# Kernel tuning notes

Hardware: AMD Instinct MI355X
Metric: run time of the kernel (lower is better)

## Reference

```python
import jax, jax.numpy as jnp
import numpy as np


def setup_inputs() -> dict:
    key = jax.random.key(0)
    ks = jax.random.split(key, 6)
    b, t, s, qu, vu, d = 8, 64, 512, 512, 512, 512
    return {
        "query": jax.random.normal(ks[0], (b, t, qu), jnp.float32),
        "value": jax.random.normal(ks[1], (b, s, vu), jnp.float32),
        "mask": jax.random.randint(ks[2], (b, s), 0, 2).astype(bool),
        "W1_w": jax.random.normal(ks[3], (qu, d), jnp.float32) * (1.0 / np.sqrt(qu)),
        "W1_b": jnp.zeros((d,), jnp.float32),
        "W2_w": jax.random.normal(ks[4], (vu, d), jnp.float32) * (1.0 / np.sqrt(vu)),
        "W2_b": jnp.zeros((d,), jnp.float32),
        "scale": jax.random.normal(ks[5], (d,), jnp.float32) * 0.05,
    }


def reference(query, value, mask, W1_w, W1_b, W2_w, W2_b, scale):
    # Dense projections
    q = jnp.einsum('btq,qd->btd', query, W1_w) + W1_b   # [b,t,d]
    k = jnp.einsum('bsv,vd->bsd', value, W2_w) + W2_b   # [b,s,d]
    # Additive (Bahdanau) score with learned scale vector (Keras use_scale=True)
    # scores[b,t,s] = sum_d scale[d] * tanh(q[b,t,d] + k[b,s,d])
    scores = jnp.einsum('btsd,d->bts', jnp.tanh(q[:, :, None, :] + k[:, None, :, :]), scale)
    # Mask over source positions (value mask); query mask is all-ones (no-op)
    scores = jnp.where(mask[:, None, :], scores, jnp.float32(-1e9))
    attention_weights = jax.nn.softmax(scores, axis=-1)   # [b,t,s]
    context_vector = jnp.einsum('bts,bsv->btv', attention_weights, value)  # [b,t,vu]
    return context_vector, attention_weights
```

## Files before the change

### kernel.cpp

```cpp
#include <hip/hip_runtime.h>
#include <hip/hip_bf16.h>
#include <hip/hip_fp16.h>

#define B_  8
#define T_  64
#define S_  512
#define D_  512

#define QN (512 * 512)
#define KN (4096 * 512)

#define TLOG2E 2.8853900817779268f
#define LOG2E  1.4426950408889634f

typedef __attribute__((ext_vector_type(8))) short bf16x8;
typedef __attribute__((ext_vector_type(4))) float f32x4;

__device__ __forceinline__ unsigned int pk2(float a, float b) {
    float2 f; f.x = a; f.y = b;
    __hip_bfloat162 h = __float22bfloat162_rn(f);
    return *(unsigned int*)&h;
}
__device__ __forceinline__ unsigned int pkh(float a, float b) {
    __half2 h = __floats2half2_rn(a, b);
    return *(unsigned int*)&h;
}
__device__ __forceinline__ float2 up2(unsigned int u) {
    __half2 h = *(__half2*)&u;
    return __half22float2(h);
}

__global__ __launch_bounds__(256) void mfma_gemm(
    const float* __restrict__ query, const float* __restrict__ value,
    const float* __restrict__ W1, const float* __restrict__ W2,
    const float* __restrict__ b1, const float* __restrict__ b2,
    float* __restrict__ qproj, unsigned short* __restrict__ kTb,
    unsigned short* __restrict__ vh)
{
    __shared__ __align__(16) unsigned short Ab[2][64][72];
    __shared__ __align__(16) unsigned short Bs[2][64][72];

    const int x = blockIdx.x;
    const int tid  = threadIdx.x;

    if (x >= 576) {
        const int c = x - 576;
        const float* src = value + (size_t)c * 128 * 512;
        unsigned short* dst = vh + (size_t)c * 128 * 512;
#pragma unroll 4
        for (int i = 0; i < 64; ++i) {
            const int f = i * 256 + tid;
            float4 v4 = *(const float4*)(src + (size_t)f * 4);
            uint2 o; o.x = pkh(v4.x, v4.y); o.y = pkh(v4.z, v4.w);
            *(uint2*)(dst + (size_t)f * 4) = o;
        }
        return;
    }

    const float *A, *W;
    int tm, tn;
    bool isq;
    if (x < 512) {
        tm = (x & 7) * 8 + ((x >> 3) & 7);
        tn = x >> 6;
        A = value; W = W2; isq = false;
    } else {
        int r = x - 512;
        tm = r >> 3; tn = r & 7;
        A = query; W = W1; isq = true;
    }

    const int lane = tid & 63;
    const int wid  = tid >> 6;
    const int wm = (wid & 1) * 32, wn = (wid >> 1) * 32;
    const int fm = lane & 15, fq = lane >> 4;

    f32x4 acc00 = {0.f, 0.f, 0.f, 0.f};
    f32x4 acc01 = acc00, acc10 = acc00, acc11 = acc00;

    const int ar = tid >> 2;
    const int kc = (tid & 3) * 16;
    const float* Ag = A + (size_t)(tm * 64 + ar) * 512 + kc;
    const int c0 = (tid & 15) * 4;
    const int kp = (tid >> 4) * 2;
    const float* Wg = W + (size_t)kp * 512 + tn * 64 + c0;

    float4 av0, av1, av2, av3;
    float4 wv0, wv1, wv2, wv3;

#define LOADT(KOFF) do {                                                      \
        av0 = *(const float4*)(Ag + (KOFF));                                  \
        av1 = *(const float4*)(Ag + (KOFF) + 4);                              \
        av2 = *(const float4*)(Ag + (KOFF) + 8);                              \
        av3 = *(const float4*)(Ag + (KOFF) + 12);                             \
        wv0 = *(const float4*)(Wg + (size_t)(KOFF) * 512);                    \
        wv1 = *(const float4*)(Wg + (size_t)(KOFF) * 512 + 512);              \
        wv2 = *(const float4*)(Wg + (size_t)((KOFF) + 32) * 512);             \
        wv3 = *(const float4*)(Wg + (size_t)((KOFF) + 32) * 512 + 512);       \
    } while (0)

#define STAGE(BUF) do {                                                       \
        uint4 p0, p1;                                                         \
        p0.x = pk2(av0.x, av0.y); p0.y = pk2(av0.z, av0.w);                   \
        p0.z = pk2(av1.x, av1.y); p0.w = pk2(av1.z, av1.w);                   \
        p1.x = pk2(av2.x, av2.y); p1.y = pk2(av2.z, av2.w);                   \
        p1.z = pk2(av3.x, av3.y); p1.w = pk2(av3.z, av3.w);                   \
        *(uint4*)&Ab[BUF][ar][kc]     = p0;                                   \
        *(uint4*)&Ab[BUF][ar][kc + 8] = p1;                                   \
        *(unsigned int*)&Bs[BUF][c0 + 0][kp]      = pk2(wv0.x, wv1.x);        \
        *(unsigned int*)&Bs[BUF][c0 + 1][kp]      = pk2(wv0.y, wv1.y);        \
        *(unsigned int*)&Bs[BUF][c0 + 2][kp]      = pk2(wv0.z, wv1.z);        \
        *(unsigned int*)&Bs[BUF][c0 + 3][kp]      = pk2(wv0.w, wv1.w);        \
        *(unsigned int*)&Bs[BUF][c0 + 0][kp + 32] = pk2(wv2.x, wv3.x);        \
        *(unsigned int*)&Bs[BUF][c0 + 1][kp + 32] = pk2(wv2.y, wv3.y);        \
        *(unsigned int*)&Bs[BUF][c0 + 2][kp + 32] = pk2(wv2.z, wv3.z);        \
        *(unsigned int*)&Bs[BUF][c0 + 3][kp + 32] = pk2(wv2.w, wv3.w);        \
    } while (0)

    LOADT(0);
    STAGE(0);
    LOADT(64);
    __syncthreads();

    for (int i = 0; i < 8; ++i) {
        const int cur = i & 1, nxt = cur ^ 1;
        bf16x8 a0, a1, b0, b1v;
#pragma unroll
        for (int kk = 0; kk < 64; kk += 32) {
            a0  = *(const bf16x8*)&Ab[cur][wm + fm][kk + fq * 8];
            a1  = *(const bf16x8*)&Ab[cur][wm + 16 + fm][kk + fq * 8];
            b0  = *(const bf16x8*)&Bs[cur][wn + fm][kk + fq * 8];
            b1v = *(const bf16x8*)&Bs[cur][wn + 16 + fm][kk + fq * 8];
            acc00 = __builtin_amdgcn_mfma_f32_16x16x32_bf16(a0, b0,  acc00, 0, 0, 0);
            acc01 = __builtin_amdgcn_mfma_f32_16x16x32_bf16(a0, b1v, acc01, 0, 0, 0);
            acc10 = __builtin_amdgcn_mfma_f32_16x16x32_bf16(a1, b0,  acc10, 0, 0, 0);
            acc11 = __builtin_amdgcn_mfma_f32_16x16x32_bf16(a1, b1v, acc11, 0, 0, 0);
        }
        if (i < 7) {
            STAGE(nxt);
            const int kn = ((i + 2) & 7) * 64;
            LOADT(kn);
        }
        __syncthreads();
    }
#undef STAGE
#undef LOADT

    const int n0 = tn * 64 + wn + fm;
    const int n1 = n0 + 16;
    const int m0 = tm * 64 + wm + fq * 4;
    if (isq) {
        float bias0 = b1[n0] + b2[n0];
        float bias1 = b1[n1] + b2[n1];
#pragma unroll
        for (int r = 0; r < 4; ++r) {
            qproj[(size_t)(m0 + r) * 512 + n0]      = (acc00[r] + bias0) * TLOG2E;
            qproj[(size_t)(m0 + r) * 512 + n1]      = (acc01[r] + bias1) * TLOG2E;
            qproj[(size_t)(m0 + 16 + r) * 512 + n0] = (acc10[r] + bias0) * TLOG2E;
            qproj[(size_t)(m0 + 16 + r) * 512 + n1] = (acc11[r] + bias1) * TLOG2E;
        }
    } else {
        const int bb = m0 >> 9;
        const int sl = m0 & 511;
        unsigned short* kb = kTb + (size_t)(bb * 512) * 512;
#define EX2(V) __builtin_amdgcn_exp2f((V) * TLOG2E)
        uint2 o;
        o.x = pkh(EX2(acc00[0]), EX2(acc00[1]));
        o.y = pkh(EX2(acc00[2]), EX2(acc00[3]));
        *(uint2*)(kb + (size_t)n0 * 512 + sl) = o;
        o.x = pkh(EX2(acc10[0]), EX2(acc10[1]));
        o.y = pkh(EX2(acc10[2]), EX2(acc10[3]));
        *(uint2*)(kb + (size_t)n0 * 512 + sl + 16) = o;
        o.x = pkh(EX2(acc01[0]), EX2(acc01[1]));
        o.y = pkh(EX2(acc01[2]), EX2(acc01[3]));
        *(uint2*)(kb + (size_t)n1 * 512 + sl) = o;
        o.x = pkh(EX2(acc11[0]), EX2(acc11[1]));
        o.y = pkh(EX2(acc11[2]), EX2(acc11[3]));
        *(uint2*)(kb + (size_t)n1 * 512 + sl + 16) = o;
#undef EX2
    }
}

__global__ __launch_bounds__(1024) void fused_attn(
    const float* __restrict__ qproj, const unsigned short* __restrict__ kTb,
    const int*   __restrict__ mask,  const float* __restrict__ scale,
    const unsigned short* __restrict__ vh,
    float* __restrict__ ctx, float* __restrict__ attn)
{
    const int blk = blockIdx.x;
    const int b  = blk & 7;
    const int tp = blk >> 3;
    const size_t row0 = (size_t)(b * T_ + tp * 2);

    __shared__ __align__(16) float q0A[512];
    __shared__ __align__(16) float dA[512];
    __shared__ __align__(16) float cA[512];
    __shared__ __align__(16) float4 pex[4][256];
    __shared__ __align__(16) float2 wp2[512];
    __shared__ __align__(16) float4 part[2][8][128];
    __shared__ float2 red2[16];

    const int tid  = threadIdx.x;
    const int lane = tid & 63;
    const int wid  = tid >> 6;

    if (tid < 512) {
        float q0v = qproj[row0 * D_ + tid];
        float q1v = qproj[(row0 + 1) * D_ + tid];
        q0A[tid] = __builtin_amdgcn_exp2f(q0v);
        dA[tid]  = __builtin_amdgcn_exp2f(q1v - q0v);
        cA[tid]  = scale[tid];
    }
    __syncthreads();

    const int sp  = tid & 255;
    const int dq  = tid >> 8;
    const int dlo = dq * 128;
    const unsigned short* kb = kTb + ((size_t)(b * 512 + dlo)) * 512 + sp * 2;

    float p00 = 0.f, p10 = 0.f, p01 = 0.f, p11 = 0.f;

    unsigned int nf0 = *(const unsigned int*)(kb);
    unsigned int nf1 = *(const unsigned int*)(kb + 512);
    unsigned int nf2 = *(const unsigned int*)(kb + 1024);
    unsigned int nf3 = *(const unsigned int*)(kb + 1536);

#define SC2(KU, EQ, DV, CV) do {                                              \
        float2 ek = up2(KU);                                                  \
        float e0 = (EQ) * ek.x;                                               \
        float e1 = (EQ) * ek.y;                                               \
        float Av = e0 + 1.0f;                                                 \
        float Bv = fmaf(e0, (DV), 1.0f);                                      \
        float Cv = e1 + 1.0f;                                                 \
        float Dv = fmaf(e1, (DV), 1.0f);                                      \
        float ab = Av * Bv, cd = Cv * Dv;                                     \
        float r  = __builtin_amdgcn_rcpf(ab * cd);                            \
        float rab = cd * r, rcd = ab * r;                                     \
        p00 = fmaf((CV), Bv * rab, p00);                                      \
        p10 = fmaf((CV), Av * rab, p10);                                      \
        p01 = fmaf((CV), Dv * rcd, p01);                                      \
        p11 = fmaf((CV), Cv * rcd, p11);                                      \
    } while (0)

    for (int g = 0; g < 32; ++g) {
        unsigned int kf0 = nf0, kf1 = nf1, kf2 = nf2, kf3 = nf3;
        const unsigned short* nb = kb + (size_t)(((g + 1) & 31) * 4) * 512;
        nf0 = *(const unsigned int*)(nb);
        nf1 = *(const unsigned int*)(nb + 512);
        nf2 = *(const unsigned int*)(nb + 1024);
        nf3 = *(const unsigned int*)(nb + 1536);
        const int d0 = dlo + g * 4;
        float4 q4 = *(const float4*)&q0A[d0];
        float4 dl = *(const float4*)&dA[d0];
        float4 c4 = *(const float4*)&cA[d0];
        SC2(kf0, q4.x, dl.x, c4.x);
        SC2(kf1, q4.y, dl.y, c4.y);
        SC2(kf2, q4.z, dl.z, c4.z);
        SC2(kf3, q4.w, dl.w, c4.w);
    }
#undef SC2

    {
        float4 pq; pq.x = p00; pq.y = p10; pq.z = p01; pq.w = p11;
        pex[dq][sp] = pq;
    }
    __syncthreads();

    float e0 = 0.f, e1 = 0.f;
    if (tid < 512) {
        const int s = tid;
        const int s2 = s >> 1;
        const bool odd = (s & 1) != 0;
        float4 r0 = pex[0][s2], r1 = pex[1][s2];
        float4 r2 = pex[2][s2], r3 = pex[3][s2];
        float pt0 = odd ? ((r0.z + r1.z) + (r2.z + r3.z))
                        : ((r0.x + r1.x) + (r2.x + r3.x));
        float pt1 = odd ? ((r0.w + r1.w) + (r2.w + r3.w))
                        : ((r0.y + r1.y) + (r2.y + r3.y));
        const int m = mask[b * S_ + s];
        if (m) {
            e0 = __builtin_amdgcn_exp2f(-TLOG2E * pt0);
            e1 = __builtin_amdgcn_exp2f(-TLOG2E * pt1);
        }
        float2 sm; sm.x = e0; sm.y = e1;
#pragma unroll
        for (int off = 32; off >= 1; off >>= 1) {
            sm.x += __shfl_xor(sm.x, off);
            sm.y += __shfl_xor(sm.y, off);
        }
        if (lane == 0) red2[wid] = sm;
    }
    __syncthreads();

    if (tid < 512) {
        const int s = tid;
        float2 SS = red2[0];
#pragma unroll
        for (int i = 1; i < 8; ++i) {
            SS.x += red2[i].x;
            SS.y += red2[i].y;
        }
        const float w0 = e0 * __builtin_amdgcn_rcpf(SS.x);
        const float w1 = e1 * __builtin_amdgcn_rcpf(SS.y);
        float2 wpair; wpair.x = w0; wpair.y = w1;
        wp2[s] = wpair;
        attn[row0 * S_ + s]       = w0;
        attn[(row0 + 1) * S_ + s] = w1;
    }
    __syncthreads();

    const int g  = tid >> 7;
    const int v4 = tid & 127;
    const unsigned short* vb = vh + ((size_t)(b * S_) + g * 64) * D_ + v4 * 4;
    float4 a0; a0.x = 0.f; a0.y = 0.f; a0.z = 0.f; a0.w = 0.f;
    float4 a1 = a0;
#pragma unroll 4
    for (int i = 0; i < 64; ++i) {
        float2 w = wp2[g * 64 + i];
        if (w.x == 0.f && w.y == 0.f) continue;
        uint2 u = *(const uint2*)(vb + (size_t)i * D_);
        float2 lo = up2(u.x), hi = up2(u.y);
        a0.x = fmaf(w.x, lo.x, a0.x); a0.y = fmaf(w.x, lo.y, a0.y);
        a0.z = fmaf(w.x, hi.x, a0.z); a0.w = fmaf(w.x, hi.y, a0.w);
        a1.x = fmaf(w.y, lo.x, a1.x); a1.y = fmaf(w.y, lo.y, a1.y);
        a1.z = fmaf(w.y, hi.x, a1.z); a1.w = fmaf(w.y, hi.y, a1.w);
    }
    part[0][g][v4] = a0;
    part[1][g][v4] = a1;
    __syncthreads();
    if (tid < 256) {
        const int t = tid >> 7, v = tid & 127;
        float4 o; o.x = 0.f; o.y = 0.f; o.z = 0.f; o.w = 0.f;
#pragma unroll
        for (int gg = 0; gg < 8; ++gg) {
            float4 p = part[t][gg][v];
            o.x += p.x; o.y += p.y; o.z += p.z; o.w += p.w;
        }
        *(float4*)(ctx + (row0 + t) * D_ + v * 4) = o;
    }
}

extern "C" void kernel_launch(void* const* d_in, const int* in_sizes, int n_in,
                              void* d_out, int out_size, void* d_ws, size_t ws_size,
                              hipStream_t stream) {
    const float* query = (const float*)d_in[0];
    const float* value = (const float*)d_in[1];
    const int*   mask  = (const int*)  d_in[2];
    const float* W1w   = (const float*)d_in[3];
    const float* W1b   = (const float*)d_in[4];
    const float* W2w   = (const float*)d_in[5];
    const float* W2b   = (const float*)d_in[6];
    const float* scale = (const float*)d_in[7];

    float* ctx  = (float*)d_out;
    float* attn = (float*)d_out + (size_t)B_ * T_ * D_;

    float* qproj = (float*)d_ws;
    unsigned short* kTb = (unsigned short*)(qproj + (size_t)QN);
    unsigned short* vh  = kTb + (size_t)KN;

    mfma_gemm<<<608, 256, 0, stream>>>(query, value, W1w, W2w, W1b, W2b,
                                       qproj, kTb, vh);
    fused_attn<<<256, 1024, 0, stream>>>(qproj, kTb, mask, scale, vh,
                                         ctx, attn);
}
```

Measured before the change: 127.9 us.

## Compact masked positions via ballot and prefetch V rows; use direct reciprocals

The context loop now visits only unmasked source positions. It builds a compacted per-wave list of positions and weights with ballot and popcount, and prefetches V rows two iterations ahead, replacing the branchy skip over zero weights. Separately, the score inner macro drops the shared-reciprocal trick and uses four separate rcp instructions instead of one rcp plus extra multiplies. This trades more transcendental ops in the hot loop for fewer multiplies, and adds some LDS bookkeeping for the compaction.

```diff
diff --git a/kernel.cpp b/kernel.cpp
--- a/kernel.cpp
+++ b/kernel.cpp
@@ -196,8 +196,10 @@
     __shared__ __align__(16) float dA[512];
     __shared__ __align__(16) float cA[512];
     __shared__ __align__(16) float4 pex[4][256];
-    __shared__ __align__(16) float2 wp2[512];
     __shared__ __align__(16) float4 part[2][8][128];
+    __shared__ __align__(16) float2 wc[8][64];
+    __shared__ int  sidc[8][64];
+    __shared__ int  cntA[8];
     __shared__ float2 red2[16];
 
     const int tid  = threadIdx.x;
@@ -228,18 +230,13 @@
 #define SC2(KU, EQ, DV, CV) do {                                              \
         float2 ek = up2(KU);                                                  \
         float e0 = (EQ) * ek.x;                                               \
+        float ra = __builtin_amdgcn_rcpf(e0 + 1.0f);                          \
+        float rb = __builtin_amdgcn_rcpf(fmaf(e0, (DV), 1.0f));               \
+        p00 = fmaf((CV), ra, p00); p10 = fmaf((CV), rb, p10);                 \
         float e1 = (EQ) * ek.y;                                               \
-        float Av = e0 + 1.0f;                                                 \
-        float Bv = fmaf(e0, (DV), 1.0f);                                      \
-        float Cv = e1 + 1.0f;                                                 \
-        float Dv = fmaf(e1, (DV), 1.0f);                                      \
-        float ab = Av * Bv, cd = Cv * Dv;                                     \
-        float r  = __builtin_amdgcn_rcpf(ab * cd);                            \
-        float rab = cd * r, rcd = ab * r;                                     \
-        p00 = fmaf((CV), Bv * rab, p00);                                      \
-        p10 = fmaf((CV), Av * rab, p10);                                      \
-        p01 = fmaf((CV), Dv * rcd, p01);                                      \
-        p11 = fmaf((CV), Cv * rcd, p11);                                      \
+        float rc = __builtin_amdgcn_rcpf(e1 + 1.0f);                          \
+        float rd = __builtin_amdgcn_rcpf(fmaf(e1, (DV), 1.0f));               \
+        p01 = fmaf((CV), rc, p01); p11 = fmaf((CV), rd, p11);                 \
     } while (0)
 
     for (int g = 0; g < 32; ++g) {
@@ -267,6 +264,7 @@
     __syncthreads();
 
     float e0 = 0.f, e1 = 0.f;
+    int   m = 0, rank = 0;
     if (tid < 512) {
         const int s = tid;
         const int s2 = s >> 1;
@@ -277,11 +275,15 @@
                         : ((r0.x + r1.x) + (r2.x + r3.x));
         float pt1 = odd ? ((r0.w + r1.w) + (r2.w + r3.w))
                         : ((r0.y + r1.y) + (r2.y + r3.y));
-        const int m = mask[b * S_ + s];
+        m = mask[b * S_ + s];
         if (m) {
             e0 = __builtin_amdgcn_exp2f(-TLOG2E * pt0);
             e1 = __builtin_amdgcn_exp2f(-TLOG2E * pt1);
         }
+        unsigned long long bal = __ballot(m != 0);
+        rank = __popcll(bal & ((1ull << lane) - 1ull));
+        if (lane == 0) cntA[wid] = (int)__popcll(bal);
+        if (m) sidc[wid][rank] = lane;
         float2 sm; sm.x = e0; sm.y = e1;
 #pragma unroll
         for (int off = 32; off >= 1; off >>= 1) {
@@ -302,8 +304,10 @@
         }
         const float w0 = e0 * __builtin_amdgcn_rcpf(SS.x);
         const float w1 = e1 * __builtin_amdgcn_rcpf(SS.y);
-        float2 wpair; wpair.x = w0; wpair.y = w1;
-        wp2[s] = wpair;
+        if (m) {
+            float2 wpair; wpair.x = w0; wpair.y = w1;
+            wc[wid][rank] = wpair;
+        }
         attn[row0 * S_ + s]       = w0;
         attn[(row0 + 1) * S_ + s] = w1;
     }
@@ -311,14 +315,29 @@
 
     const int g  = tid >> 7;
     const int v4 = tid & 127;
-    const unsigned short* vb = vh + ((size_t)(b * S_) + g * 64) * D_ + v4 * 4;
+    const unsigned short* vbase = vh + ((size_t)(b * S_) + g * 64) * D_ + v4 * 4;
     float4 a0; a0.x = 0.f; a0.y = 0.f; a0.z = 0.f; a0.w = 0.f;
     float4 a1 = a0;
-#pragma unroll 4
-    for (int i = 0; i < 64; ++i) {
-        float2 w = wp2[g * 64 + i];
-        if (w.x == 0.f && w.y == 0.f) continue;
-        uint2 u = *(const uint2*)(vb + (size_t)i * D_);
+
+    const int cnt = cntA[g];
+    float2 w0r, w1r; uint2 u0r, u1r;
+    w0r.x = 0.f; w0r.y = 0.f; w1r = w0r;
+    u0r.x = 0u; u0r.y = 0u; u1r = u0r;
+    if (0 < cnt) {
+        int so = sidc[g][0]; w0r = wc[g][0];
+        u0r = *(const uint2*)(vbase + (size_t)so * D_);
+    }
+    if (1 < cnt) {
+        int so = sidc[g][1]; w1r = wc[g][1];
+        u1r = *(const uint2*)(vbase + (size_t)so * D_);
+    }
+    for (int r = 0; r < cnt; ++r) {
+        float2 w = w0r; uint2 u = u0r;
+        w0r = w1r; u0r = u1r;
+        if (r + 2 < cnt) {
+            int so = sidc[g][r + 2]; w1r = wc[g][r + 2];
+            u1r = *(const uint2*)(vbase + (size_t)so * D_);
+        }
         float2 lo = up2(u.x), hi = up2(u.y);
         a0.x = fmaf(w.x, lo.x, a0.x); a0.y = fmaf(w.x, lo.y, a0.y);
         a0.z = fmaf(w.x, hi.x, a0.z); a0.w = fmaf(w.x, hi.y, a0.w);
```

After: 125.5 us. Within noise of the previous version (-1.9%).

## Process one query row per block instead of two in fused attention

Applied to the files above, without the earlier changes.

Restructures the fused attention kernel so each block handles a single query row, doubling the grid to 512 blocks. The tanh score uses one reciprocal per element instead of a shared reciprocal over four terms computed from two rows. This is meant to raise parallelism and reduce register pressure and per-thread arithmetic, but it doubles K and V reads across blocks and raises reciprocal count. It also drops the skip of zero-weight rows in the context accumulation.

```diff
diff --git a/kernel.cpp b/kernel.cpp
--- a/kernel.cpp
+++ b/kernel.cpp
@@ -189,26 +189,23 @@
 {
     const int blk = blockIdx.x;
     const int b  = blk & 7;
-    const int tp = blk >> 3;
-    const size_t row0 = (size_t)(b * T_ + tp * 2);
-
-    __shared__ __align__(16) float q0A[512];
-    __shared__ __align__(16) float dA[512];
+    const int tr = blk >> 3;
+    const size_t row = (size_t)(b * T_ + tr);
+
+    __shared__ __align__(16) float eqA[512];
     __shared__ __align__(16) float cA[512];
-    __shared__ __align__(16) float4 pex[4][256];
-    __shared__ __align__(16) float2 wp2[512];
-    __shared__ __align__(16) float4 part[2][8][128];
-    __shared__ float2 red2[16];
+    __shared__ __align__(16) float2 pex[4][256];
+    __shared__ __align__(16) float  wp[512];
+    __shared__ __align__(16) float4 part[8][128];
+    __shared__ float red[8];
 
     const int tid  = threadIdx.x;
     const int lane = tid & 63;
     const int wid  = tid >> 6;
 
     if (tid < 512) {
-        float q0v = qproj[row0 * D_ + tid];
-        float q1v = qproj[(row0 + 1) * D_ + tid];
-        q0A[tid] = __builtin_amdgcn_exp2f(q0v);
-        dA[tid]  = __builtin_amdgcn_exp2f(q1v - q0v);
+        float qv = qproj[row * D_ + tid];
+        eqA[tid] = __builtin_amdgcn_exp2f(qv);
         cA[tid]  = scale[tid];
     }
     __syncthreads();
@@ -218,28 +215,21 @@
     const int dlo = dq * 128;
     const unsigned short* kb = kTb + ((size_t)(b * 512 + dlo)) * 512 + sp * 2;
 
-    float p00 = 0.f, p10 = 0.f, p01 = 0.f, p11 = 0.f;
+    float p0 = 0.f, p1 = 0.f;
 
     unsigned int nf0 = *(const unsigned int*)(kb);
     unsigned int nf1 = *(const unsigned int*)(kb + 512);
     unsigned int nf2 = *(const unsigned int*)(kb + 1024);
     unsigned int nf3 = *(const unsigned int*)(kb + 1536);
 
-#define SC2(KU, EQ, DV, CV) do {                                              \
+#define SC1(KU, EQ, CV) do {                                                  \
         float2 ek = up2(KU);                                                  \
         float e0 = (EQ) * ek.x;                                               \
+        float ra = __builtin_amdgcn_rcpf(e0 + 1.0f);                          \
+        p0 = fmaf((CV), ra, p0);                                              \
         float e1 = (EQ) * ek.y;                                               \
-        float Av = e0 + 1.0f;                                                 \
-        float Bv = fmaf(e0, (DV), 1.0f);                                      \
-        float Cv = e1 + 1.0f;                                                 \
-        float Dv = fmaf(e1, (DV), 1.0f);                                      \
-        float ab = Av * Bv, cd = Cv * Dv;                                     \
-        float r  = __builtin_amdgcn_rcpf(ab * cd);                            \
-        float rab = cd * r, rcd = ab * r;                                     \
-        p00 = fmaf((CV), Bv * rab, p00);                                      \
-        p10 = fmaf((CV), Av * rab, p10);                                      \
-        p01 = fmaf((CV), Dv * rcd, p01);                                      \
-        p11 = fmaf((CV), Cv * rcd, p11);                                      \
+        float rc = __builtin_amdgcn_rcpf(e1 + 1.0f);                          \
+        p1 = fmaf((CV), rc, p1);                                              \
     } while (0)
 
     for (int g = 0; g < 32; ++g) {
@@ -250,93 +240,75 @@
         nf2 = *(const unsigned int*)(nb + 1024);
         nf3 = *(const unsigned int*)(nb + 1536);
         const int d0 = dlo + g * 4;
-        float4 q4 = *(const float4*)&q0A[d0];
-        float4 dl = *(const float4*)&dA[d0];
+        float4 q4 = *(const float4*)&eqA[d0];
         float4 c4 = *(const float4*)&cA[d0];
-        SC2(kf0, q4.x, dl.x, c4.x);
-        SC2(kf1, q4.y, dl.y, c4.y);
-        SC2(kf2, q4.z, dl.z, c4.z);
-        SC2(kf3, q4.w, dl.w, c4.w);
-    }
-#undef SC2
+        SC1(kf0, q4.x, c4.x);
+        SC1(kf1, q4.y, c4.y);
+        SC1(kf2, q4.z, c4.z);
+        SC1(kf3, q4.w, c4.w);
+    }
+#undef SC1
 
     {
-        float4 pq; pq.x = p00; pq.y = p10; pq.z = p01; pq.w = p11;
+        float2 pq; pq.x = p0; pq.y = p1;
         pex[dq][sp] = pq;
     }
     __syncthreads();
 
-    float e0 = 0.f, e1 = 0.f;
+    float e = 0.f;
     if (tid < 512) {
         const int s = tid;
         const int s2 = s >> 1;
         const bool odd = (s & 1) != 0;
-        float4 r0 = pex[0][s2], r1 = pex[1][s2];
-        float4 r2 = pex[2][s2], r3 = pex[3][s2];
-        float pt0 = odd ? ((r0.z + r1.z) + (r2.z + r3.z))
-                        : ((r0.x + r1.x) + (r2.x + r3.x));
-        float pt1 = odd ? ((r0.w + r1.w) + (r2.w + r3.w))
-                        : ((r0.y + r1.y) + (r2.y + r3.y));
+        float2 r0 = pex[0][s2], r1 = pex[1][s2];
+        float2 r2 = pex[2][s2], r3 = pex[3][s2];
+        float pt = odd ? ((r0.y + r1.y) + (r2.y + r3.y))
+                       : ((r0.x + r1.x) + (r2.x + r3.x));
         const int m = mask[b * S_ + s];
         if (m) {
-            e0 = __builtin_amdgcn_exp2f(-TLOG2E * pt0);
-            e1 = __builtin_amdgcn_exp2f(-TLOG2E * pt1);
-        }
-        float2 sm; sm.x = e0; sm.y = e1;
+            e = __builtin_amdgcn_exp2f(-TLOG2E * pt);
+        }
+        float sm = e;
 #pragma unroll
         for (int off = 32; off >= 1; off >>= 1) {
-            sm.x += __shfl_xor(sm.x, off);
-            sm.y += __shfl_xor(sm.y, off);
-        }
-        if (lane == 0) red2[wid] = sm;
+            sm += __shfl_xor(sm, off);
+        }
+        if (lane == 0) red[wid] = sm;
     }
     __syncthreads();
 
     if (tid < 512) {
-        const int s = tid;
-        float2 SS = red2[0];
-#pragma unroll
-        for (int i = 1; i < 8; ++i) {
-            SS.x += red2[i].x;
-            SS.y += red2[i].y;
-        }
-        const float w0 = e0 * __builtin_amdgcn_rcpf(SS.x);
-        const float w1 = e1 * __builtin_amdgcn_rcpf(SS.y);
-        float2 wpair; wpair.x = w0; wpair.y = w1;
-        wp2[s] = wpair;
-        attn[row0 * S_ + s]       = w0;
-        attn[(row0 + 1) * S_ + s] = w1;
+        float SS = red[0];
+#pragma unroll
+        for (int i = 1; i < 8; ++i) SS += red[i];
+        const float w = e * __builtin_amdgcn_rcpf(SS);
+        wp[tid] = w;
+        attn[row * S_ + tid] = w;
     }
     __syncthreads();
 
     const int g  = tid >> 7;
     const int v4 = tid & 127;
     const unsigned short* vb = vh + ((size_t)(b * S_) + g * 64) * D_ + v4 * 4;
-    float4 a0; a0.x = 0.f; a0.y = 0.f; a0.z = 0.f; a0.w = 0.f;
-    float4 a1 = a0;
+    float4 a; a.x = 0.f; a.y = 0.f; a.z = 0.f; a.w = 0.f;
 #pragma unroll 4
     for (int i = 0; i < 64; ++i) {
-        float2 w = wp2[g * 64 + i];
-        if (w.x == 0.f && w.y == 0.f) continue;
         uint2 u = *(const uint2*)(vb + (size_t)i * D_);
+        float w = wp[g * 64 + i];
         float2 lo = up2(u.x), hi = up2(u.y);
-        a0.x = fmaf(w.x, lo.x, a0.x); a0.y = fmaf(w.x, lo.y, a0.y);
-        a0.z = fmaf(w.x, hi.x, a0.z); a0.w = fmaf(w.x, hi.y, a0.w);
-        a1.x = fmaf(w.y, lo.x, a1.x); a1.y = fmaf(w.y, lo.y, a1.y);
-        a1.z = fmaf(w.y, hi.x, a1.z); a1.w = fmaf(w.y, hi.y, a1.w);
-    }
-    part[0][g][v4] = a0;
-    part[1][g][v4] = a1;
-    __syncthreads();
-    if (tid < 256) {
-        const int t = tid >> 7, v = tid & 127;
+        a.x = fmaf(w, lo.x, a.x); a.y = fmaf(w, lo.y, a.y);
+        a.z = fmaf(w, hi.x, a.z); a.w = fmaf(w, hi.y, a.w);
+    }
+    part[g][v4] = a;
+    __syncthreads();
+    if (tid < 128) {
         float4 o; o.x = 0.f; o.y = 0.f; o.z = 0.f; o.w = 0.f;
 #pragma unroll
         for (int gg = 0; gg < 8; ++gg) {
-            float4 p = part[t][gg][v];
+            float4 p = part[gg][tid];
             o.x += p.x; o.y += p.y; o.z += p.z; o.w += p.w;
         }
-        *(float4*)(ctx + (row0 + t) * D_ + v * 4) = o;
+        *(float4*)(ctx + row * D_ + tid * 4) = o;
     }
 }
 
@@ -361,6 +333,6 @@
 
     mfma_gemm<<<608, 256, 0, stream>>>(query, value, W1w, W2w, W1b, W2b,
                                        qproj, kTb, vh);
-    fused_attn<<<256, 1024, 0, stream>>>(qproj, kTb, mask, scale, vh,
+    fused_attn<<<512, 1024, 0, stream>>>(qproj, kTb, mask, scale, vh,
                                          ctx, attn);
 }
```

After: 124.0 us. 1.03x faster.
